# Kernel optimization log

Hardware: AMD Instinct MI355X
Metric: run time of the kernel (lower is better)

## Reference

```python
import jax, jax.numpy as jnp
import numpy as np

EPS = 1e-7
CURVS = (1.0, 0.8, 1.2)
SCALES = (1.0, 0.8, 0.6)


def expmap0(v, c):
    sc = jnp.sqrt(c)
    n = jnp.maximum(jnp.linalg.norm(v, axis=-1, keepdims=True), EPS)
    return jnp.tanh(sc * n) * v / (sc * n)


def projx(x, c):
    max_n = (1.0 - 1e-5) / jnp.sqrt(c)
    n = jnp.maximum(jnp.linalg.norm(x, axis=-1, keepdims=True), EPS)
    return jnp.where(n > max_n, x * (max_n / n), x)


def logmap0(x, c):
    sc = jnp.sqrt(c)
    n = jnp.maximum(jnp.linalg.norm(x, axis=-1, keepdims=True), EPS)
    a = jnp.clip(sc * n, 0.0, 1.0 - 1e-7)
    return jnp.arctanh(a) * x / (sc * n)


def hamilton(q1, q2):
    # q1, q2: [..., 4] (w,x,y,z), broadcasting allowed
    w1, x1, y1, z1 = q1[..., 0], q1[..., 1], q1[..., 2], q1[..., 3]
    w2, x2, y2, z2 = q2[..., 0], q2[..., 1], q2[..., 2], q2[..., 3]
    w = w1 * w2 - x1 * x2 - y1 * y2 - z1 * z2
    x = w1 * x2 + x1 * w2 + y1 * z2 - z1 * y2
    y = w1 * y2 - x1 * z2 + y1 * w2 + z1 * x2
    z = w1 * z2 + x1 * y2 - y1 * x2 + z1 * w2
    return jnp.stack([w, x, y, z], axis=-1)


def mlp(v, Wa, ba, Wb, bb):
    # Linear -> GELU(exact, matching torch default) -> Linear; dropout is eval-mode identity
    return jax.nn.gelu(v @ Wa.T + ba, approximate=False) @ Wb.T + bb


def setup_inputs() -> dict:
    key = jax.random.key(0)
    ks = jax.random.split(key, 24)
    f32 = jnp.float32
    B = 65536
    d = {}
    d['x'] = jax.random.normal(ks[0], (B, 784), dtype=f32)
    # input embedding 784 -> 128, then to level-0 tangent space 128 -> 64
    d['W_in'] = jax.random.normal(ks[1], (128, 784), f32) * (1.0 / np.sqrt(784))
    d['b_in'] = jnp.zeros((128,), f32)
    d['W_tan'] = jax.random.normal(ks[2], (64, 128), f32) * (1.0 / np.sqrt(128))
    d['b_tan'] = jnp.zeros((64,), f32)
    # boundary-manifold tangent points per level (init_scale=0.01 as in BoundaryManifold)
    d['bp0'] = jax.random.normal(ks[3], (5, 64), f32) * 0.01
    d['bp1'] = jax.random.normal(ks[4], (3, 4), f32) * 0.01
    d['bp2'] = jax.random.normal(ks[5], (4, 32), f32) * 0.01
    # rotation 0->1: SO(64) via matrix exponential of a skew-symmetric generator
    d['A_rot'] = jax.random.normal(ks[6], (64, 64), f32) * 0.02
    # rotation 1->2: SO(4) via pvq unit quaternions (std=0.1 init as in source)
    d['p_quat'] = jax.random.normal(ks[7], (4,), f32) * 0.1
    d['q_quat'] = jax.random.normal(ks[8], (4,), f32) * 0.1
    # inter-level MLP transform 0->1: 64 -> 32 -> 4
    d['W0a'] = jax.random.normal(ks[9], (32, 64), f32) * (1.0 / np.sqrt(64))
    d['b0a'] = jnp.zeros((32,), f32)
    d['W0b'] = jax.random.normal(ks[10], (4, 32), f32) * (1.0 / np.sqrt(32))
    d['b0b'] = jnp.zeros((4,), f32)
    # inter-level MLP transform 1->2: 4 -> 16 -> 32
    d['W1a'] = jax.random.normal(ks[11], (16, 4), f32) * (1.0 / np.sqrt(4))
    d['b1a'] = jnp.zeros((16,), f32)
    d['W1b'] = jax.random.normal(ks[12], (32, 16), f32) * (1.0 / np.sqrt(16))
    d['b1b'] = jnp.zeros((32,), f32)
    # output head: concat_tangent (64+4+32=100) -> 10
    d['W_out'] = jax.random.normal(ks[13], (10, 100), f32) * (1.0 / np.sqrt(100))
    d['b_out'] = jnp.zeros((10,), f32)
    return d


def reference(x, W_in, b_in, W_tan, b_tan, bp0, bp1, bp2, A_rot, p_quat, q_quat,
              W0a, b0a, W0b, b0b, W1a, b1a, W1b, b1b, W_out, b_out):
    h = x @ W_in.T + b_in                       # [B, 128]
    v = h @ W_tan.T + b_tan                     # [B, 64] level-0 tangent vector
    bps = (bp0, bp1, bp2)
    level_tangents = []
    carried = None                              # boundary tangent vectors transformed from prev level
    for i in range(3):
        c, s = CURVS[i], SCALES[i]
        # scaled exp/log round trip through the Poincare ball of this level
        x_hyp = projx(expmap0(v * s, c), c)
        v_tan = logmap0(x_hyp, c) / s           # [B, d_i]
        # boundary manifold: tangent -> ball -> proj -> tangent
        b_own = logmap0(projx(expmap0(bps[i], c), c), c)  # [P_i, d_i]
        bnds = b_own if carried is None else jnp.concatenate([b_own, carried], axis=0)
        # relative vectors vs boundary points, mean-aggregated
        rel_agg = v_tan.mean(axis=0, keepdims=False) * 0 + (v_tan[:, None, :] - bnds[None, :, :]).mean(axis=1)  # [B, d_i]
        level_tangents.append(v_tan)
        v_comb = v_tan + rel_agg
        if i == 0:
            R = jax.scipy.linalg.expm(A_rot - A_rot.T)   # SO(64)
            v_rot = v_comb @ R.T
            b_rot = bnds @ R.T
            v = mlp(v_rot, W0a, b0a, W0b, b0b)
            carried = mlp(b_rot, W0a, b0a, W0b, b0b)
        elif i == 1:
            p = p_quat / (jnp.linalg.norm(p_quat) + EPS)
            q = q_quat / (jnp.linalg.norm(q_quat) + EPS)
            v_rot = hamilton(hamilton(p, v_comb), q)     # pvq SO(4) rotation
            b_rot = hamilton(hamilton(p, bnds), q)
            v = mlp(v_rot, W1a, b1a, W1b, b1b)
            carried = mlp(b_rot, W1a, b1a, W1b, b1b)
    agg = jnp.concatenate(level_tangents, axis=-1)       # [B, 100] concat_tangent
    return agg @ W_out.T + b_out                         # [B, 10]
```

## Files before the change

kernel.cpp:

```cpp
#include <hip/hip_runtime.h>
#include <hip/hip_bf16.h>

typedef __attribute__((ext_vector_type(4))) float f32x4;
typedef __attribute__((ext_vector_type(2))) unsigned int u32x2;
typedef __attribute__((ext_vector_type(4))) unsigned int u32x4;
typedef __attribute__((ext_vector_type(8))) short bf16x8;

#define EPSF 1e-7f

__device__ __forceinline__ float radial_factor(float sumsq, float c, float s){
  float sc = sqrtf(c);
  float nv = sqrtf(sumsq);
  float nu = fmaxf(s*nv, EPSF);
  float th = tanhf(sc*nu);
  float r1 = th/sc;
  float maxn = (1.0f - 1e-5f)/sc;
  float r2 = fminf(r1, maxn);
  float n1 = fmaxf(r2, EPSF);
  float a  = fminf(sc*n1, 1.0f - 1e-7f);
  float r3 = 0.5f*logf((1.0f + a)/(1.0f - a));
  return r3*r2/(sc*n1*nu);
}

__device__ __forceinline__ float gelu_f(float x){
  return 0.5f*x*(1.0f + erff(x*0.70710678118654752f));
}

__device__ __forceinline__ unsigned f2bf1(float f){
  unsigned u = __float_as_uint(f);
  return (u + 0x7FFFu + ((u>>16)&1u)) >> 16;
}
__device__ __forceinline__ unsigned f2bf_pk(float lo, float hi){
  unsigned ul = f2bf1(lo);
  unsigned uh = __float_as_uint(hi);
  uh = (uh + 0x7FFFu + ((uh>>16)&1u)) & 0xFFFF0000u;
  return ul | uh;
}

__device__ __forceinline__ void gload_lds16(const void* g, void* l){
  __builtin_amdgcn_global_load_lds((const __attribute__((address_space(1))) unsigned int*)g,
                                   (__attribute__((address_space(3))) unsigned int*)l,
                                   16, 0, 0);
}

#define WS_WC     0
#define WS_BCOMB  204800
#define WS_W0AE   205056
#define WS_BROT0  213248
#define WS_BOWN0  214528
#define WS_W0AT   215808
#define WS_MB0    224000
#define WS_MB1    224256
#define WS_W1AE   224272
#define WS_ZERO   224528

__global__ __launch_bounds__(256) void prep_a(
    const float* __restrict__ W_in, const float* __restrict__ b_in,
    const float* __restrict__ W_tan, const float* __restrict__ b_tan,
    const float* __restrict__ A_rot, const float* __restrict__ W0a,
    const float* __restrict__ bp0,
    unsigned short* __restrict__ Wc, float* __restrict__ bcomb,
    float* __restrict__ W0aE, float* __restrict__ brot0, float* __restrict__ bown0)
{
  __shared__ __align__(16) float Al[64][68];
  __shared__ __align__(16) float ST[64][68];
  const int bid = blockIdx.x, t = threadIdx.x;

  if (bid < 50){
    if (bid == 0 && t < 64){
      float s = b_tan[t];
      for (int j = 0; j < 128; ++j) s += b_in[j]*W_tan[t*128+j];
      bcomb[t] = s;
    }
    const int g4 = bid*256 + t;
    const int n = g4/200, k4 = (g4 - n*200)*4;
    f32x4 s = {0.f,0.f,0.f,0.f};
    if (k4 < 784){
      for (int j = 0; j < 128; ++j){
        float wt = W_tan[n*128+j];
        f32x4 wi = *(const f32x4*)(W_in + j*784 + k4);
        s += wt*wi;
      }
    }
    u32x2 st = { f2bf_pk(s[0], s[1]), f2bf_pk(s[2], s[3]) };
    const int tsl = k4 >> 5;
    const int q   = (k4 >> 3) & 3;
    const int qp  = q ^ ((n >> 1) & 3);
    const int idx = tsl*2048 + n*32 + qp*8 + (k4 & 7);
    *(u32x2*)(Wc + idx) = st;
  } else {
    for (int m = t; m < 4096; m += 256){
      int r = m >> 6, c = m & 63;
      Al[r][c] = A_rot[m];
    }
    __syncthreads();
    for (int m = t; m < 4096; m += 256){
      int r = m >> 6, c = m & 63;
      ST[r][c] = Al[c][r] - Al[r][c];
    }
    __syncthreads();
    const int wv = t >> 6, lane = t & 63;
    const int row = (bid - 50)*4 + wv;
    if (row < 37){
      float v, sgn;
      if (row < 32){ v = W0a[row*64 + lane]; sgn = 1.f; }
      else {
        const int r = row - 32;
        float b = bp0[r*64 + lane];
        float ssq = b*b;
        #pragma unroll
        for (int d = 1; d < 64; d <<= 1) ssq += __shfl_xor(ssq, d);
        float fc = radial_factor(ssq, 1.0f, 1.0f);
        v = b*fc;
        bown0[r*64 + lane] = v;
        sgn = -1.f;
      }
      float acc = v;
      for (int k = 1; k <= 12; ++k){
        const float coef = sgn/(float)k;
        float nv = 0.f;
        #pragma unroll
        for (int m = 0; m < 64; m += 4){
          f32x4 s4 = *(const f32x4*)&ST[lane][m];
          nv += __int_as_float(__builtin_amdgcn_readlane(__float_as_int(v), m+0))*s4[0];
          nv += __int_as_float(__builtin_amdgcn_readlane(__float_as_int(v), m+1))*s4[1];
          nv += __int_as_float(__builtin_amdgcn_readlane(__float_as_int(v), m+2))*s4[2];
          nv += __int_as_float(__builtin_amdgcn_readlane(__float_as_int(v), m+3))*s4[3];
        }
        nv *= coef;
        v = nv; acc += nv;
      }
      if (row < 32) W0aE[row*64 + lane] = acc;
      else          brot0[(row-32)*64 + lane] = acc;
    }
  }
}

__global__ __launch_bounds__(256) void prep_small(
    const float* __restrict__ bp1,
    const float* __restrict__ p_quat, const float* __restrict__ q_quat,
    const float* __restrict__ b0a, const float* __restrict__ W0b, const float* __restrict__ b0b,
    const float* __restrict__ W1a,
    const float* __restrict__ W0aE, const float* __restrict__ brot0, const float* __restrict__ bown0,
    float* __restrict__ W0aT, float* __restrict__ mb0, float* __restrict__ mb1,
    float* __restrict__ W1aE, float* __restrict__ zerog)
{
  __shared__ float g[5][32];
  __shared__ float c1[5][4];
  __shared__ float fac1[3];
  __shared__ float Mq[4][4];
  const int t = threadIdx.x;

  for (int i = t; i < 2048; i += 256){
    int o = i >> 6, k = i & 63;
    W0aT[k*32 + o] = W0aE[i];
  }
  if (t >= 240) zerog[t - 240] = 0.f;
  if (t < 64){
    float s = 0.f;
    for (int r = 0; r < 5; ++r) s += bown0[r*64 + t];
    mb0[t] = s * 0.2f;
  }
  if (t < 160){
    int r = t >> 5, o = t & 31;
    float s = b0a[o];
    for (int k = 0; k < 64; ++k) s += brot0[r*64+k]*W0aE[o*64+k];
    g[r][o] = gelu_f(s);
  }
  if (t >= 192 && t < 195){
    int r = t - 192;
    float ssq = 0.f;
    for (int j = 0; j < 4; ++j){ float b = bp1[r*4+j]; ssq += b*b; }
    fac1[r] = radial_factor(ssq, 0.8f, 1.0f);
  }
  if (t == 224){
    float pw=p_quat[0],px=p_quat[1],py=p_quat[2],pz=p_quat[3];
    float n1 = sqrtf(pw*pw+px*px+py*py+pz*pz) + EPSF;
    pw/=n1; px/=n1; py/=n1; pz/=n1;
    float qw=q_quat[0],qx=q_quat[1],qy=q_quat[2],qz=q_quat[3];
    float n2 = sqrtf(qw*qw+qx*qx+qy*qy+qz*qz) + EPSF;
    qw/=n2; qx/=n2; qy/=n2; qz/=n2;
    float Lp[4][4] = {{pw,-px,-py,-pz},{px,pw,-pz,py},{py,pz,pw,-px},{pz,-py,px,pw}};
    float Rq[4][4] = {{qw,-qx,-qy,-qz},{qx,qw,qz,-qy},{qy,-qz,qw,qx},{qz,qy,-qx,qw}};
    #pragma unroll
    for (int i = 0; i < 4; ++i)
      #pragma unroll
      for (int k = 0; k < 4; ++k){
        float s = 0.f;
        #pragma unroll
        for (int m = 0; m < 4; ++m) s += Rq[i][m]*Lp[m][k];
        Mq[i][k] = s;
      }
  }
  __syncthreads();
  if (t < 20){
    int r = t >> 2, o = t & 3;
    float s = b0b[o];
    for (int k = 0; k < 32; ++k) s += g[r][k]*W0b[o*32+k];
    c1[r][o] = s;
  }
  __syncthreads();
  if (t < 4){
    float s = 0.f;
    for (int r = 0; r < 3; ++r) s += bp1[r*4+t]*fac1[r];
    for (int r = 0; r < 5; ++r) s += c1[r][t];
    mb1[t] = s * 0.125f;
  }
  if (t >= 64 && t < 128){
    int i = t - 64, o = i >> 2, kq = i & 3;
    float s = 0.f;
    #pragma unroll
    for (int j = 0; j < 4; ++j) s += W1a[o*4+j]*Mq[j][kq];
    W1aE[o*4+kq] = s;
  }
}

__global__ __launch_bounds__(256, 3) void main_fused(
    const float* __restrict__ x,
    const unsigned short* __restrict__ Wcs,
    const float* __restrict__ bcomb,
    const float* __restrict__ W0aT,
    const float* __restrict__ mb0g, const float* __restrict__ mb1g,
    const float* __restrict__ W1aEg,
    const float* __restrict__ b0a, const float* __restrict__ W0b, const float* __restrict__ b0b,
    const float* __restrict__ b1a, const float* __restrict__ W1b, const float* __restrict__ b1b,
    const float* __restrict__ Wout, const float* __restrict__ bout,
    const float* __restrict__ zerog,
    float* __restrict__ out)
{
  __shared__ __align__(16) char smem[49728];
  float* vlds   = (float*)smem;
  float* cWoutS = (float*)(smem + 19456);
  float* cbcombS= (float*)(smem + 23456);
  float* cmb0S  = (float*)(smem + 23712);
  float* cW0bS  = (float*)(smem + 23968);
  float* cW1aES = (float*)(smem + 24480);
  float* cb0aS  = (float*)(smem + 24736);
  float* cb0bS  = (float*)(smem + 24864);
  float* cmb1S  = (float*)(smem + 24880);
  float* cb1aS  = (float*)(smem + 24896);
  float* cb1bS  = (float*)(smem + 24960);
  float* cboutS = (float*)(smem + 25088);
  char*  xsB    = smem + 25152;
  char*  wcsB   = smem + 41536;
  float* gv     = (float*)(smem + 25152);
  float* g1     = (float*)(smem + 34368);
  float* cW0aTS = (float*)(smem + 39488);
  float* cW1bS  = (float*)(smem + 47680);

  const int tid = threadIdx.x;
  const size_t rowBase = (size_t)blockIdx.x * 64;

  if (tid < 64)  cbcombS[tid] = bcomb[tid];
  if (tid < 64)  cmb0S[tid] = mb0g[tid];
  if (tid < 32)  cb0aS[tid] = b0a[tid];
  if (tid < 128) cW0bS[tid] = W0b[tid];
  if (tid < 4)   { cb0bS[tid] = b0b[tid]; cmb1S[tid] = mb1g[tid]; }
  if (tid < 64)  cW1aES[tid] = W1aEg[tid];
  if (tid < 16)  cb1aS[tid] = b1a[tid];
  if (tid < 32)  cb1bS[tid] = b1b[tid];
  if (tid < 10)  cboutS[tid] = bout[tid];
  for (int i = tid; i < 1000; i += 256) cWoutS[i] = Wout[i];

  const int lane = tid & 63;
  const int w    = tid >> 6;
  const int wr   = w >> 1, wc = w & 1;
  const int lr   = lane & 15, lkg = lane >> 4;

  const int row8 = lane >> 3;
  const int qs   = lane & 7;
  const int qoff = qs ^ row8;
  const float* xsrcA = x + (rowBase + (size_t)(8*w     + row8))*784 + qoff*4;
  const float* xsrcB = x + (rowBase + (size_t)(8*(w+4) + row8))*784 + qoff*4;
  const unsigned short* wsrc = Wcs + (16*w + (lane>>2))*32 + (lane&3)*8;

  const int rA0 = wr*32 + lr;
  const int sA0 = (2*lkg)     ^ (lr & 7);
  const int sA1 = (2*lkg + 1) ^ (lr & 7);
  const int offA00 = rA0*128 + sA0*16;
  const int offA01 = rA0*128 + sA1*16;
  const int rB0 = wc*32 + lr;
  const int sB  = lkg ^ ((rB0 >> 1) & 3);
  const int offB0 = rB0*64 + sB*16;

#define STAGE(slab, buf) do{                                                   \
    const int ks_ = (slab)*32;                                                 \
    char* xd_ = xsB  + (buf)*8192;                                             \
    char* wd_ = wcsB + (buf)*4096;                                             \
    const float* sa_ = (ks_ + qoff*4 < 784) ? (xsrcA + ks_) : zerog;           \
    const float* sb_ = (ks_ + qoff*4 < 784) ? (xsrcB + ks_) : zerog;           \
    gload_lds16(sa_, xd_ + w*1024);                                            \
    gload_lds16(sb_, xd_ + (w+4)*1024);                                        \
    gload_lds16(wsrc + (slab)*2048, wd_ + w*1024);                             \
  }while(0)

  STAGE(0, 0);
  __syncthreads();

  f32x4 acc00 = {}, acc01 = {}, acc10 = {}, acc11 = {};
  for (int t = 0; t < 25; ++t){
    const int cur = t & 1;
    if (t < 24) STAGE(t+1, cur^1);
    const char* xb = xsB  + cur*8192;
    const char* wb = wcsB + cur*4096;
    f32x4 a00 = *(const f32x4*)(xb + offA00);
    f32x4 a01 = *(const f32x4*)(xb + offA01);
    f32x4 a10 = *(const f32x4*)(xb + offA00 + 2048);
    f32x4 a11 = *(const f32x4*)(xb + offA01 + 2048);
    bf16x8 b0 = *(const bf16x8*)(wb + offB0);
    bf16x8 b1 = *(const bf16x8*)(wb + offB0 + 1024);
    u32x4 pk0 = { f2bf_pk(a00[0],a00[1]), f2bf_pk(a00[2],a00[3]),
                  f2bf_pk(a01[0],a01[1]), f2bf_pk(a01[2],a01[3]) };
    u32x4 pk1 = { f2bf_pk(a10[0],a10[1]), f2bf_pk(a10[2],a10[3]),
                  f2bf_pk(a11[0],a11[1]), f2bf_pk(a11[2],a11[3]) };
    bf16x8 af0 = __builtin_bit_cast(bf16x8, pk0);
    bf16x8 af1 = __builtin_bit_cast(bf16x8, pk1);
    acc00 = __builtin_amdgcn_mfma_f32_16x16x32_bf16(af0, b0, acc00, 0, 0, 0);
    acc01 = __builtin_amdgcn_mfma_f32_16x16x32_bf16(af0, b1, acc01, 0, 0, 0);
    acc10 = __builtin_amdgcn_mfma_f32_16x16x32_bf16(af1, b0, acc10, 0, 0, 0);
    acc11 = __builtin_amdgcn_mfma_f32_16x16x32_bf16(af1, b1, acc11, 0, 0, 0);
    __syncthreads();
  }
#undef STAGE

  {
    f32x4 accA[2][2] = { {acc00, acc01}, {acc10, acc11} };
    #pragma unroll
    for (int fi = 0; fi < 2; ++fi){
      #pragma unroll
      for (int fj = 0; fj < 2; ++fj){
        const int col = wc*32 + fj*16 + lr;
        const int r0  = wr*32 + fi*16 + lkg*4;
        const float bc = cbcombS[col];
        #pragma unroll
        for (int j = 0; j < 4; ++j)
          vlds[(r0 + j)*76 + col] = accA[fi][fj][j] + bc;
      }
    }
  }
  for (int i = tid; i < 2048; i += 256) cW0aTS[i] = W0aT[i];
  for (int i = tid; i < 512;  i += 256) cW1bS[i]  = W1b[i];
  __syncthreads();

  const int row = tid >> 2, p4 = tid & 3;

  {
    f32x4 rv[4];
    float* vptr = &vlds[row*76 + p4*16];
    #pragma unroll
    for (int i = 0; i < 4; ++i) rv[i] = ((const f32x4*)vptr)[i];
    float ssq = 0.f;
    #pragma unroll
    for (int i = 0; i < 4; ++i)
      ssq += rv[i][0]*rv[i][0] + rv[i][1]*rv[i][1] + rv[i][2]*rv[i][2] + rv[i][3]*rv[i][3];
    ssq += __shfl_xor(ssq, 1); ssq += __shfl_xor(ssq, 2);
    const float fac = radial_factor(ssq, 1.0f, 1.0f);
    #pragma unroll
    for (int i = 0; i < 4; ++i){ rv[i] *= fac; ((f32x4*)vptr)[i] = rv[i]; }
  }
  __syncthreads();

  {
    const int og = p4;
    float a0o[8];
    #pragma unroll
    for (int j = 0; j < 8; ++j) a0o[j] = cb0aS[og*8 + j];
    #pragma unroll 4
    for (int k = 0; k < 64; k += 4){
      f32x4 vtv = *(const f32x4*)&vlds[row*76 + k];
      f32x4 mm  = *(const f32x4*)&cmb0S[k];
      #pragma unroll
      for (int u = 0; u < 4; ++u){
        const float vc = 2.f*vtv[u] - mm[u];
        const f32x4* wp = (const f32x4*)&cW0aTS[(k+u)*32 + og*8];
        f32x4 w0 = wp[0], w1 = wp[1];
        #pragma unroll
        for (int j = 0; j < 4; ++j){ a0o[j] += w0[j]*vc; a0o[4+j] += w1[j]*vc; }
      }
    }
    #pragma unroll
    for (int j = 0; j < 8; ++j) gv[row*36 + og*8 + j] = gelu_f(a0o[j]);
  }
  __syncthreads();

  {
    const int o1 = p4;
    float a1 = cb0bS[o1];
    #pragma unroll
    for (int k = 0; k < 32; k += 4){
      f32x4 gg = *(const f32x4*)&gv[row*36 + k];
      f32x4 ww = *(const f32x4*)&cW0bS[o1*32 + k];
      a1 += gg[0]*ww[0] + gg[1]*ww[1] + gg[2]*ww[2] + gg[3]*ww[3];
    }
    float ss1 = a1*a1;
    ss1 += __shfl_xor(ss1, 1); ss1 += __shfl_xor(ss1, 2);
    const float f1v = radial_factor(ss1, 0.8f, 0.8f);
    const float vt1 = a1*f1v;
    vlds[row*76 + 64 + o1] = vt1;
    vlds[row*76 + 68 + o1] = 2.f*vt1 - cmb1S[o1];
  }
  __syncthreads();

  {
    const f32x4 vc1 = *(const f32x4*)&vlds[row*76 + 68];
    #pragma unroll
    for (int j = 0; j < 4; ++j){
      const int o = p4*4 + j;
      float s1 = cb1aS[o] + cW1aES[o*4+0]*vc1[0] + cW1aES[o*4+1]*vc1[1]
                          + cW1aES[o*4+2]*vc1[2] + cW1aES[o*4+3]*vc1[3];
      g1[row*20 + o] = gelu_f(s1);
    }
  }
  __syncthreads();

  {
    float v2[8]; float ss2 = 0.f;
    #pragma unroll
    for (int j = 0; j < 8; ++j){
      const int o = p4*8 + j;
      float s = cb1bS[o];
      #pragma unroll
      for (int k = 0; k < 16; k += 4){
        f32x4 gg = *(const f32x4*)&g1[row*20 + k];
        f32x4 ww = *(const f32x4*)&cW1bS[o*16 + k];
        s += gg[0]*ww[0] + gg[1]*ww[1] + gg[2]*ww[2] + gg[3]*ww[3];
      }
      v2[j] = s; ss2 += s*s;
    }
    ss2 += __shfl_xor(ss2, 1); ss2 += __shfl_xor(ss2, 2);
    const float f2v = radial_factor(ss2, 1.2f, 0.6f);
    #pragma unroll
    for (int j = 0; j < 8; ++j) gv[row*36 + p4*8 + j] = v2[j]*f2v;
  }
  __syncthreads();

  for (int idx = tid; idx < 640; idx += 256){
    const int r6 = idx/10, o = idx - r6*10;
    float s = cboutS[o];
    const float* wrow = &cWoutS[o*100];
    const float* vrow = &vlds[r6*76];
    #pragma unroll 4
    for (int k = 0; k < 68; k += 4){
      f32x4 a = *(const f32x4*)(vrow + k);
      f32x4 b = *(const f32x4*)(wrow + k);
      s += a[0]*b[0] + a[1]*b[1] + a[2]*b[2] + a[3]*b[3];
    }
    const float* v2row = &gv[r6*36];
    #pragma unroll 4
    for (int k = 0; k < 32; k += 4){
      f32x4 a = *(const f32x4*)(v2row + k);
      f32x4 b = *(const f32x4*)(wrow + 68 + k);
      s += a[0]*b[0] + a[1]*b[1] + a[2]*b[2] + a[3]*b[3];
    }
    out[(rowBase + (size_t)r6)*10 + o] = s;
  }
}

extern "C" void kernel_launch(void* const* d_in, const int* in_sizes, int n_in,
                              void* d_out, int out_size, void* d_ws, size_t ws_size,
                              hipStream_t stream)
{
  (void)n_in; (void)out_size; (void)ws_size;
  const float* x      = (const float*)d_in[0];
  const float* W_in   = (const float*)d_in[1];
  const float* b_in   = (const float*)d_in[2];
  const float* W_tan  = (const float*)d_in[3];
  const float* b_tan  = (const float*)d_in[4];
  const float* bp0    = (const float*)d_in[5];
  const float* bp1    = (const float*)d_in[6];
  const float* A_rot  = (const float*)d_in[8];
  const float* p_quat = (const float*)d_in[9];
  const float* q_quat = (const float*)d_in[10];
  const float* W0a    = (const float*)d_in[11];
  const float* b0a    = (const float*)d_in[12];
  const float* W0b    = (const float*)d_in[13];
  const float* b0b    = (const float*)d_in[14];
  const float* W1a    = (const float*)d_in[15];
  const float* b1a    = (const float*)d_in[16];
  const float* W1b    = (const float*)d_in[17];
  const float* b1b    = (const float*)d_in[18];
  const float* W_out  = (const float*)d_in[19];
  const float* b_out  = (const float*)d_in[20];

  char* ws = (char*)d_ws;
  unsigned short* Wcs = (unsigned short*)(ws + WS_WC);
  float* bcomb = (float*)(ws + WS_BCOMB);
  float* W0aE  = (float*)(ws + WS_W0AE);
  float* brot0 = (float*)(ws + WS_BROT0);
  float* bown0 = (float*)(ws + WS_BOWN0);
  float* W0aT  = (float*)(ws + WS_W0AT);
  float* mb0   = (float*)(ws + WS_MB0);
  float* mb1   = (float*)(ws + WS_MB1);
  float* W1aE  = (float*)(ws + WS_W1AE);
  float* zerog = (float*)(ws + WS_ZERO);

  const int Brows = in_sizes[0] / 784;
  const int nblk  = Brows / 64;

  prep_a<<<60, 256, 0, stream>>>(W_in, b_in, W_tan, b_tan, A_rot, W0a, bp0,
                                 Wcs, bcomb, W0aE, brot0, bown0);
  prep_small<<<1, 256, 0, stream>>>(bp1, p_quat, q_quat, b0a, W0b, b0b, W1a,
                                    W0aE, brot0, bown0, W0aT, mb0, mb1, W1aE, zerog);
  main_fused<<<nblk, 256, 0, stream>>>(x, Wcs, bcomb, W0aT, mb0, mb1, W1aE,
                                       b0a, W0b, b0b, b1a, W1b, b1b,
                                       W_out, b_out, zerog, (float*)d_out);
}
```

Before: 85.64 us.

## Split fused kernel into GEMM kernel and per-row epilogue kernel

Splits the monolithic fused kernel into a streaming GEMM kernel that writes the 64-wide tangent vectors to a global workspace, and a second kernel that reads them back and runs the hyperbolic maps, small MLPs and output projection. The GEMM kernel uses much less shared memory and asks for higher occupancy, so more waves can hide the latency of streaming x. The cost is an extra global round trip of B×64 floats, a second launch, and reading W_out straight from global memory.

```diff
diff --git a/kernel.cpp b/kernel.cpp
--- a/kernel.cpp
+++ b/kernel.cpp
@@ -53,6 +53,7 @@
 #define WS_MB1    224256
 #define WS_W1AE   224272
 #define WS_ZERO   224528
+#define WS_V      225280
 
 __global__ __launch_bounds__(256) void prep_a(
     const float* __restrict__ W_in, const float* __restrict__ b_in,
@@ -215,57 +216,23 @@
   }
 }
 
-__global__ __launch_bounds__(256, 3) void main_fused(
+__global__ __launch_bounds__(256, 6) void gemm_v(
     const float* __restrict__ x,
     const unsigned short* __restrict__ Wcs,
     const float* __restrict__ bcomb,
-    const float* __restrict__ W0aT,
-    const float* __restrict__ mb0g, const float* __restrict__ mb1g,
-    const float* __restrict__ W1aEg,
-    const float* __restrict__ b0a, const float* __restrict__ W0b, const float* __restrict__ b0b,
-    const float* __restrict__ b1a, const float* __restrict__ W1b, const float* __restrict__ b1b,
-    const float* __restrict__ Wout, const float* __restrict__ bout,
     const float* __restrict__ zerog,
-    float* __restrict__ out)
+    float* __restrict__ v)
 {
-  __shared__ __align__(16) char smem[49728];
-  float* vlds   = (float*)smem;
-  float* cWoutS = (float*)(smem + 19456);
-  float* cbcombS= (float*)(smem + 23456);
-  float* cmb0S  = (float*)(smem + 23712);
-  float* cW0bS  = (float*)(smem + 23968);
-  float* cW1aES = (float*)(smem + 24480);
-  float* cb0aS  = (float*)(smem + 24736);
-  float* cb0bS  = (float*)(smem + 24864);
-  float* cmb1S  = (float*)(smem + 24880);
-  float* cb1aS  = (float*)(smem + 24896);
-  float* cb1bS  = (float*)(smem + 24960);
-  float* cboutS = (float*)(smem + 25088);
-  char*  xsB    = smem + 25152;
-  char*  wcsB   = smem + 41536;
-  float* gv     = (float*)(smem + 25152);
-  float* g1     = (float*)(smem + 34368);
-  float* cW0aTS = (float*)(smem + 39488);
-  float* cW1bS  = (float*)(smem + 47680);
-
-  const int tid = threadIdx.x;
-  const size_t rowBase = (size_t)blockIdx.x * 64;
-
-  if (tid < 64)  cbcombS[tid] = bcomb[tid];
-  if (tid < 64)  cmb0S[tid] = mb0g[tid];
-  if (tid < 32)  cb0aS[tid] = b0a[tid];
-  if (tid < 128) cW0bS[tid] = W0b[tid];
-  if (tid < 4)   { cb0bS[tid] = b0b[tid]; cmb1S[tid] = mb1g[tid]; }
-  if (tid < 64)  cW1aES[tid] = W1aEg[tid];
-  if (tid < 16)  cb1aS[tid] = b1a[tid];
-  if (tid < 32)  cb1bS[tid] = b1b[tid];
-  if (tid < 10)  cboutS[tid] = bout[tid];
-  for (int i = tid; i < 1000; i += 256) cWoutS[i] = Wout[i];
-
+  __shared__ __align__(16) char smem[24576];
+  char* xsB  = smem;
+  char* wcsB = smem + 16384;
+
+  const int tid  = threadIdx.x;
   const int lane = tid & 63;
   const int w    = tid >> 6;
   const int wr   = w >> 1, wc = w & 1;
   const int lr   = lane & 15, lkg = lane >> 4;
+  const size_t rowBase = (size_t)blockIdx.x * 64;
 
   const int row8 = lane >> 3;
   const int qs   = lane & 7;
@@ -326,20 +293,62 @@
   {
     f32x4 accA[2][2] = { {acc00, acc01}, {acc10, acc11} };
     #pragma unroll
-    for (int fi = 0; fi < 2; ++fi){
+    for (int fj = 0; fj < 2; ++fj){
+      const int col = wc*32 + fj*16 + lr;
+      const float bc = bcomb[col];
       #pragma unroll
-      for (int fj = 0; fj < 2; ++fj){
-        const int col = wc*32 + fj*16 + lr;
-        const int r0  = wr*32 + fi*16 + lkg*4;
-        const float bc = cbcombS[col];
+      for (int fi = 0; fi < 2; ++fi){
+        const int r0 = wr*32 + fi*16 + lkg*4;
         #pragma unroll
         for (int j = 0; j < 4; ++j)
-          vlds[(r0 + j)*76 + col] = accA[fi][fj][j] + bc;
-      }
-    }
+          v[(rowBase + (size_t)(r0 + j))*64 + col] = accA[fi][fj][j] + bc;
+      }
+    }
+  }
+}
+
+__global__ __launch_bounds__(256, 4) void row_phase(
+    const float* __restrict__ vg,
+    const float* __restrict__ W0aT,
+    const float* __restrict__ mb0g, const float* __restrict__ mb1g,
+    const float* __restrict__ W1aEg,
+    const float* __restrict__ b0a, const float* __restrict__ W0b, const float* __restrict__ b0b,
+    const float* __restrict__ b1a, const float* __restrict__ W1b, const float* __restrict__ b1b,
+    const float* __restrict__ Wout, const float* __restrict__ bout,
+    float* __restrict__ out)
+{
+  __shared__ __align__(16) char smem[38304];
+  float* vlds   = (float*)smem;
+  float* gv     = (float*)(smem + 19456);
+  float* cW0aTS = (float*)(smem + 28672);
+  float* g1     = (float*)(smem + 28672);
+  float* cW1bS  = (float*)(smem + 33792);
+  float* cmb0S  = (float*)(smem + 36864);
+  float* cW0bS  = (float*)(smem + 37120);
+  float* cW1aES = (float*)(smem + 37632);
+  float* cb0aS  = (float*)(smem + 37888);
+  float* cb0bS  = (float*)(smem + 38016);
+  float* cmb1S  = (float*)(smem + 38032);
+  float* cb1aS  = (float*)(smem + 38048);
+  float* cb1bS  = (float*)(smem + 38112);
+  float* cboutS = (float*)(smem + 38240);
+
+  const int tid = threadIdx.x;
+  const size_t rowBase = (size_t)blockIdx.x * 64;
+
+  for (int i = tid; i < 1024; i += 256){
+    const int r = i >> 4, seg = i & 15;
+    *(f32x4*)&vlds[r*76 + seg*4] = *(const f32x4*)(vg + (rowBase + (size_t)r)*64 + seg*4);
   }
   for (int i = tid; i < 2048; i += 256) cW0aTS[i] = W0aT[i];
-  for (int i = tid; i < 512;  i += 256) cW1bS[i]  = W1b[i];
+  if (tid < 64)  cmb0S[tid] = mb0g[tid];
+  if (tid < 32)  cb0aS[tid] = b0a[tid];
+  if (tid < 128) cW0bS[tid] = W0b[tid];
+  if (tid < 4)   { cb0bS[tid] = b0b[tid]; cmb1S[tid] = mb1g[tid]; }
+  if (tid < 64)  cW1aES[tid] = W1aEg[tid];
+  if (tid < 16)  cb1aS[tid] = b1a[tid];
+  if (tid < 32)  cb1bS[tid] = b1b[tid];
+  if (tid < 10)  cboutS[tid] = bout[tid];
   __syncthreads();
 
   const int row = tid >> 2, p4 = tid & 3;
@@ -401,6 +410,7 @@
   }
   __syncthreads();
 
+  for (int i = tid; i < 512; i += 256) cW1bS[i] = W1b[i];
   {
     const f32x4 vc1 = *(const f32x4*)&vlds[row*76 + 68];
     #pragma unroll
@@ -437,7 +447,7 @@
   for (int idx = tid; idx < 640; idx += 256){
     const int r6 = idx/10, o = idx - r6*10;
     float s = cboutS[o];
-    const float* wrow = &cWoutS[o*100];
+    const float* wrow = Wout + o*100;
     const float* vrow = &vlds[r6*76];
     #pragma unroll 4
     for (int k = 0; k < 68; k += 4){
@@ -493,6 +503,7 @@
   float* mb1   = (float*)(ws + WS_MB1);
   float* W1aE  = (float*)(ws + WS_W1AE);
   float* zerog = (float*)(ws + WS_ZERO);
+  float* vbuf  = (float*)(ws + WS_V);
 
   const int Brows = in_sizes[0] / 784;
   const int nblk  = Brows / 64;
@@ -501,7 +512,8 @@
                                  Wcs, bcomb, W0aE, brot0, bown0);
   prep_small<<<1, 256, 0, stream>>>(bp1, p_quat, q_quat, b0a, W0b, b0b, W1a,
                                     W0aE, brot0, bown0, W0aT, mb0, mb1, W1aE, zerog);
-  main_fused<<<nblk, 256, 0, stream>>>(x, Wcs, bcomb, W0aT, mb0, mb1, W1aE,
-                                       b0a, W0b, b0b, b1a, W1b, b1b,
-                                       W_out, b_out, zerog, (float*)d_out);
-}
+  gemm_v<<<nblk, 256, 0, stream>>>(x, Wcs, bcomb, zerog, vbuf);
+  row_phase<<<nblk, 256, 0, stream>>>(vbuf, W0aT, mb0, mb1, W1aE,
+                                      b0a, W0b, b0b, b1a, W1b, b1b,
+                                      W_out, b_out, (float*)d_out);
+}
```

New measurement: 88.41 us. 3.2% more time.
